# Optimization experiments

Measured on AMD Instinct MI355X. Metric: run time of the kernel, lower is better.

## Reference

```python
import jax, jax.numpy as jnp
from jax import lax
import numpy as np

B, T, D, H, K = 16, 1024, 1024, 1024, 2


def setup_inputs() -> dict:
    key = jax.random.key(0)
    k1, k2 = jax.random.split(key, 2)
    inputs = jax.random.normal(k1, (B, T, D), dtype=jnp.float32)
    # small init so tanh/sigmoid gates are not saturated
    conv_w = jax.random.normal(k2, (3 * H, D, K), dtype=jnp.float32) * 0.02
    conv_b = jnp.zeros((3 * H,), dtype=jnp.float32)
    return {"inputs": inputs, "conv_w": conv_w, "conv_b": conv_b, "layer_idx": 0}


def _qrnn_forward(inputs, conv_w, conv_b):
    k = conv_w.shape[-1]
    h = conv_w.shape[0] // 3
    # causal conv1d: pad (k-1) on the left of the time axis
    x = jnp.transpose(inputs, (0, 2, 1))                 # [B, D, T]
    x = jnp.pad(x, ((0, 0), (0, 0), (k - 1, 0)))         # [B, D, T+k-1]
    gates = lax.conv_general_dilated(
        x, conv_w, window_strides=(1,), padding="VALID",
        dimension_numbers=("NCH", "OIH", "NCH"))         # [B, 3H, T]
    gates = jnp.transpose(gates, (0, 2, 1)) + conv_b     # [B, T, 3H]
    Z = jnp.tanh(gates[..., :h])
    F = jax.nn.sigmoid(gates[..., h:2 * h])
    O = jax.nn.sigmoid(gates[..., 2 * h:])

    # fo-pooling recurrence: c_t = f_t * c_{t-1} + (1 - f_t) * z_t, c_0 = 0
    def step(c, zf):
        z, f = zf
        c_ = f * c + (1.0 - f) * z
        return c_, c_

    c0 = jnp.zeros((Z.shape[0], h), dtype=Z.dtype)
    zT = jnp.transpose(Z, (1, 0, 2))                     # [T, B, H]
    fT = jnp.transpose(F, (1, 0, 2))
    _, cT = lax.scan(step, c0, (zT, fT))                 # [T, B, H]
    c_time = jnp.transpose(cT, (1, 0, 2))                # [B, T, H]
    h_time = O * c_time
    return c_time, h_time


def reference(inputs, conv_w, conv_b, layer_idx):
    # layer_idx=0 with state=None, memory=None: no conv_linear memory term,
    # no attention, zero initial cell state.
    return _qrnn_forward(inputs, conv_w, conv_b)
```

## Files before the change

### kernel.cpp

```cpp
#include <hip/hip_runtime.h>

#define BB 16
#define TT 1024
#define DD 1024
#define HH 1024
#define NN 3072
#define KK 2048
#define MM (BB * TT)
#define TP (TT + 1)
#define NCH 32
#define TC  32
#define PLANE (1u << 24)

typedef __attribute__((ext_vector_type(8))) short short8;
typedef __attribute__((ext_vector_type(4))) float float4v;

__device__ __forceinline__ unsigned short f2bf(float f) {
    unsigned int u = __float_as_uint(f);
    u += 0x7fffu + ((u >> 16) & 1u);
    return (unsigned short)(u >> 16);
}
__device__ __forceinline__ float bf2f(unsigned short s) {
    return __uint_as_float(((unsigned int)s) << 16);
}

__device__ __forceinline__ void gload_lds16(const unsigned short* g, unsigned short* l) {
    __builtin_amdgcn_global_load_lds(
        (const __attribute__((address_space(1))) unsigned int*)(g),
        (__attribute__((address_space(3))) unsigned int*)(l),
        16, 0, 0);
}

__global__ __launch_bounds__(256) void pack_x_kernel(const float* __restrict__ x,
                                                     unsigned short* __restrict__ xpad) {
    int i = blockIdx.x * 256 + threadIdx.x;
    int total = BB * TP * (DD / 4);
    if (i >= total) return;
    int d4  = i & (DD / 4 - 1);
    int row = i >> 8;
    int b  = row / TP;
    int tp = row - b * TP;
    float4 v = make_float4(0.f, 0.f, 0.f, 0.f);
    if (tp > 0)
        v = ((const float4*)x)[(((size_t)(b * TT + tp - 1)) << 8) + d4];
    ushort4 r4;
    r4.x = f2bf(v.x); r4.y = f2bf(v.y); r4.z = f2bf(v.z); r4.w = f2bf(v.w);
    *(ushort4*)(xpad + (((size_t)row) << 10) + (d4 << 2)) = r4;
}

__global__ __launch_bounds__(256) void pack_w_kernel(const float* __restrict__ w,
                                                     unsigned short* __restrict__ Bt) {
    int i = blockIdx.x * 256 + threadIdx.x;
    if (i >= NN * DD) return;
    int n = i >> 10, d = i & 1023;
    float2 v = ((const float2*)w)[i];
    Bt[(size_t)n * KK + d]       = f2bf(v.x);
    Bt[(size_t)n * KK + DD + d]  = f2bf(v.y);
}


#define STAGE_TILE(ASN, BSN, KT) do {                                          \
    const int tap_ = (KT) >> 4;                                                \
    const size_t aoff_ = aSrc + (((size_t)tap_) << 10) + (((KT) & 15) << 6);   \
    const size_t boff_ = bSrc + (((size_t)(KT)) << 6);                         \
    gload_lds16(xpad + aoff_,                 (ASN) + ldsStage);               \
    gload_lds16(xpad + aoff_ + (64u << 10),   (ASN) + ldsStage + 4096);        \
    gload_lds16(xpad + aoff_ + (128u << 10),  (ASN) + ldsStage + 8192);        \
    gload_lds16(xpad + aoff_ + (192u << 10),  (ASN) + ldsStage + 12288);       \
    gload_lds16(Btw + boff_,                  (BSN) + ldsStage);               \
    gload_lds16(Btw + boff_ + (64u << 11),    (BSN) + ldsStage + 4096);        \
    gload_lds16(Btw + boff_ + (128u << 11),   (BSN) + ldsStage + 8192);        \
    gload_lds16(Btw + boff_ + (192u << 11),   (BSN) + ldsStage + 12288);       \
} while (0)

#define MFMA16(P, AA, AB, AC, AD) do {                                         \
    __builtin_amdgcn_s_setprio(1);                                             \
    acc[2*(P)  ][0] = __builtin_amdgcn_mfma_f32_16x16x32_bf16(AA, b00, acc[2*(P)  ][0], 0, 0, 0); \
    acc[2*(P)+1][0] = __builtin_amdgcn_mfma_f32_16x16x32_bf16(AB, b00, acc[2*(P)+1][0], 0, 0, 0); \
    acc[2*(P)  ][1] = __builtin_amdgcn_mfma_f32_16x16x32_bf16(AA, b10, acc[2*(P)  ][1], 0, 0, 0); \
    acc[2*(P)+1][1] = __builtin_amdgcn_mfma_f32_16x16x32_bf16(AB, b10, acc[2*(P)+1][1], 0, 0, 0); \
    acc[2*(P)  ][2] = __builtin_amdgcn_mfma_f32_16x16x32_bf16(AA, b20, acc[2*(P)  ][2], 0, 0, 0); \
    acc[2*(P)+1][2] = __builtin_amdgcn_mfma_f32_16x16x32_bf16(AB, b20, acc[2*(P)+1][2], 0, 0, 0); \
    acc[2*(P)  ][3] = __builtin_amdgcn_mfma_f32_16x16x32_bf16(AA, b30, acc[2*(P)  ][3], 0, 0, 0); \
    acc[2*(P)+1][3] = __builtin_amdgcn_mfma_f32_16x16x32_bf16(AB, b30, acc[2*(P)+1][3], 0, 0, 0); \
    acc[2*(P)  ][0] = __builtin_amdgcn_mfma_f32_16x16x32_bf16(AC, b01, acc[2*(P)  ][0], 0, 0, 0); \
    acc[2*(P)+1][0] = __builtin_amdgcn_mfma_f32_16x16x32_bf16(AD, b01, acc[2*(P)+1][0], 0, 0, 0); \
    acc[2*(P)  ][1] = __builtin_amdgcn_mfma_f32_16x16x32_bf16(AC, b11, acc[2*(P)  ][1], 0, 0, 0); \
    acc[2*(P)+1][1] = __builtin_amdgcn_mfma_f32_16x16x32_bf16(AD, b11, acc[2*(P)+1][1], 0, 0, 0); \
    acc[2*(P)  ][2] = __builtin_amdgcn_mfma_f32_16x16x32_bf16(AC, b21, acc[2*(P)  ][2], 0, 0, 0); \
    acc[2*(P)+1][2] = __builtin_amdgcn_mfma_f32_16x16x32_bf16(AD, b21, acc[2*(P)+1][2], 0, 0, 0); \
    acc[2*(P)  ][3] = __builtin_amdgcn_mfma_f32_16x16x32_bf16(AC, b31, acc[2*(P)  ][3], 0, 0, 0); \
    acc[2*(P)+1][3] = __builtin_amdgcn_mfma_f32_16x16x32_bf16(AD, b31, acc[2*(P)+1][3], 0, 0, 0); \
    __builtin_amdgcn_s_setprio(0);                                             \
} while (0)

#define TILE(ASC, BSC, ASN, BSN, KTN, DOSTAGE) do {                            \
    const unsigned short* aP_ = (ASC) + aRowRd;                                \
    const unsigned short* bP_ = (BSC) + bRowRd;                                \
    short8 b00 = *(const short8*)(bP_ +    0 + pch0);                          \
    short8 b10 = *(const short8*)(bP_ + 1024 + pch0);                          \
    short8 b20 = *(const short8*)(bP_ + 2048 + pch0);                          \
    short8 b30 = *(const short8*)(bP_ + 3072 + pch0);                          \
    short8 aAx = *(const short8*)(aP_ +    0 + pch0);                          \
    short8 aBx = *(const short8*)(aP_ + 1024 + pch0);                          \
    short8 b01 = *(const short8*)(bP_ +    0 + pch1);                          \
    short8 b11 = *(const short8*)(bP_ + 1024 + pch1);                          \
    short8 b21 = *(const short8*)(bP_ + 2048 + pch1);                          \
    short8 b31 = *(const short8*)(bP_ + 3072 + pch1);                          \
    short8 aCx = *(const short8*)(aP_ +    0 + pch1);                          \
    short8 aDx = *(const short8*)(aP_ + 1024 + pch1);                          \
    if (DOSTAGE) { STAGE_TILE(ASN, BSN, KTN); }                                \
    MFMA16(0, aAx, aBx, aCx, aDx);                                             \
    aAx = *(const short8*)(aP_ + 2048 + pch0);                                 \
    aBx = *(const short8*)(aP_ + 3072 + pch0);                                 \
    aCx = *(const short8*)(aP_ + 2048 + pch1);                                 \
    aDx = *(const short8*)(aP_ + 3072 + pch1);                                 \
    MFMA16(1, aAx, aBx, aCx, aDx);                                             \
    aAx = *(const short8*)(aP_ + 4096 + pch0);                                 \
    aBx = *(const short8*)(aP_ + 5120 + pch0);                                 \
    aCx = *(const short8*)(aP_ + 4096 + pch1);                                 \
    aDx = *(const short8*)(aP_ + 5120 + pch1);                                 \
    MFMA16(2, aAx, aBx, aCx, aDx);                                             \
    aAx = *(const short8*)(aP_ + 6144 + pch0);                                 \
    aBx = *(const short8*)(aP_ + 7168 + pch0);                                 \
    aCx = *(const short8*)(aP_ + 6144 + pch1);                                 \
    aDx = *(const short8*)(aP_ + 7168 + pch1);                                 \
    MFMA16(3, aAx, aBx, aCx, aDx);                                             \
    __syncthreads();                                                           \
} while (0)

__global__ __launch_bounds__(512, 2) void gemm_gates_kernel(const unsigned short* __restrict__ xpad,
                                                            const unsigned short* __restrict__ Btw,
                                                            const float* __restrict__ bias,
                                                            unsigned short* __restrict__ zT) {
    extern __shared__ unsigned short lds[];
    unsigned short* As0 = lds;
    unsigned short* As1 = lds + 16384;
    unsigned short* Bs0 = lds + 32768;
    unsigned short* Bs1 = lds + 49152;

    const int tid  = threadIdx.x;
    const int lane = tid & 63;
    const int w    = tid >> 6;
    const int wm   = w >> 2;
    const int wn   = w & 3;
    const int mrow = lane & 15;
    const int quad = lane >> 4;

    const int m0 = blockIdx.x << 8;
    const int n0 = blockIdx.y << 8;
    const int bidx = m0 >> 10;
    const int t0   = m0 & 1023;

    const int rr  = tid >> 3;
    const int cc8 = (((tid & 7) ^ (rr & 7)) << 3);
    const size_t aSrc = (((size_t)(bidx * TP + t0 + rr)) << 10) + cc8;
    const size_t bSrc = (((size_t)(n0 + rr)) << 11) + cc8;
    const int ldsStage = (rr << 6) + ((tid & 7) << 3);

    const int pch0 = ((quad ^ (lane & 7)) << 3);
    const int pch1 = (((4 | quad) ^ (lane & 7)) << 3);
    const int aRowRd = ((wm << 7) + mrow) << 6;
    const int bRowRd = ((wn << 6) + mrow) << 6;

    float4v acc[8][4];
#pragma unroll
    for (int i = 0; i < 8; ++i)
#pragma unroll
        for (int j = 0; j < 4; ++j) acc[i][j] = (float4v)0.0f;

    STAGE_TILE(As0, Bs0, 0);
    __syncthreads();

#pragma unroll 1
    for (int jt = 0; jt < 30; jt += 2) {
        TILE(As0, Bs0, As1, Bs1, jt + 1, 1);
        TILE(As1, Bs1, As0, Bs0, jt + 2, 1);
    }
    TILE(As0, Bs0, As1, Bs1, 31, 1);
    TILE(As1, Bs1, As0, Bs0, 0, 0);

    unsigned short* Ts = lds;
    const bool isZ = (n0 < HH);
    float bv[4];
#pragma unroll
    for (int ng = 0; ng < 4; ++ng) bv[ng] = bias[n0 + (wn << 6) + (ng << 4) + mrow];

#pragma unroll
    for (int g = 0; g < 8; ++g) {
#pragma unroll
        for (int ng = 0; ng < 4; ++ng) {
            const int nloc = (wn << 6) + (ng << 4) + mrow;
            const int m0l  = (wm << 7) + (g << 4) + (quad << 2);
            float v0 = acc[g][ng][0] + bv[ng];
            float v1 = acc[g][ng][1] + bv[ng];
            float v2 = acc[g][ng][2] + bv[ng];
            float v3 = acc[g][ng][3] + bv[ng];
            float g0, g1, g2, g3;
            if (isZ) {
                g0 = 2.0f * __builtin_amdgcn_rcpf(1.0f + __expf(-2.0f * v0)) - 1.0f;
                g1 = 2.0f * __builtin_amdgcn_rcpf(1.0f + __expf(-2.0f * v1)) - 1.0f;
                g2 = 2.0f * __builtin_amdgcn_rcpf(1.0f + __expf(-2.0f * v2)) - 1.0f;
                g3 = 2.0f * __builtin_amdgcn_rcpf(1.0f + __expf(-2.0f * v3)) - 1.0f;
            } else {
                g0 = __builtin_amdgcn_rcpf(1.0f + __expf(-v0));
                g1 = __builtin_amdgcn_rcpf(1.0f + __expf(-v1));
                g2 = __builtin_amdgcn_rcpf(1.0f + __expf(-v2));
                g3 = __builtin_amdgcn_rcpf(1.0f + __expf(-v3));
            }
            unsigned int d0 = (unsigned int)f2bf(g0) | ((unsigned int)f2bf(g1) << 16);
            unsigned int d1 = (unsigned int)f2bf(g2) | ((unsigned int)f2bf(g3) << 16);
            const int chunk = (m0l >> 3) ^ (nloc & 31);
            *(uint2*)(Ts + nloc * 256 + (chunk << 3) + (m0l & 7)) = make_uint2(d0, d1);
        }
    }
    __syncthreads();

    const int gate = n0 >> 10;
    unsigned short* plane = zT + ((size_t)gate << 24);
    const int cl = lane & 31;
#pragma unroll
    for (int p = 0; p < 16; ++p) {
        const int np = (p << 4) + (tid >> 5);
        short8 vv = *(const short8*)(Ts + np * 256 + ((cl ^ (np & 31)) << 3));
        const int h = (n0 & 1023) + np;
        const size_t dst = ((((size_t)((bidx << 10) | h)) << 10) | (unsigned)(t0 + (cl << 3)));
        *(short8*)(plane + dst) = vv;
    }
}


__global__ __launch_bounds__(256) void scan_summary_kernel(const unsigned short* __restrict__ zT,
                                                           float* __restrict__ P,
                                                           float* __restrict__ S) {
    int g = blockIdx.x * 256 + threadIdx.x;
    int h = g & 1023;
    int b = (g >> 10) & 15;
    int j = g >> 14;
    const unsigned short* zp = zT + ((((size_t)((b << 10) | h)) << 10) + j * TC);
    const unsigned short* fp = zp + PLANE;
    short8 zv[4], fv[4];
#pragma unroll
    for (int q = 0; q < 4; ++q) {
        zv[q] = *(const short8*)(zp + q * 8);
        fv[q] = *(const short8*)(fp + q * 8);
    }
    float c = 0.f, pr = 1.f;
#pragma unroll
    for (int q = 0; q < 4; ++q)
#pragma unroll
        for (int k = 0; k < 8; ++k) {
            float z = bf2f((unsigned short)zv[q][k]);
            float f = bf2f((unsigned short)fv[q][k]);
            c = fmaf(f, c, (1.0f - f) * z);
            pr *= f;
        }
    int o = (j << 14) | (b << 10) | h;
    P[o] = pr;
    S[o] = c;
}

__global__ __launch_bounds__(256) void scan_prefix_kernel(const float* __restrict__ P,
                                                          const float* __restrict__ S,
                                                          float* __restrict__ Cin) {
    int idx = blockIdx.x * 256 + threadIdx.x;
    float c = 0.f;
#pragma unroll
    for (int j = 0; j < NCH; ++j) {
        int o = (j << 14) + idx;
        Cin[o] = c;
        c = fmaf(P[o], c, S[o]);
    }
}

__global__ __launch_bounds__(256) void scan_apply_kernel(const unsigned short* __restrict__ zT,
                                                         const float* __restrict__ Cin,
                                                         float* __restrict__ out) {
    int g = blockIdx.x * 256 + threadIdx.x;
    int h = g & 1023;
    int b = (g >> 10) & 15;
    int j = g >> 14;
    const unsigned short* zp = zT + ((((size_t)((b << 10) | h)) << 10) + j * TC);
    const unsigned short* fp = zp + PLANE;
    const unsigned short* op = zp + 2 * (size_t)PLANE;
    short8 zv[4], fv[4], ov[4];
#pragma unroll
    for (int q = 0; q < 4; ++q) {
        zv[q] = *(const short8*)(zp + q * 8);
        fv[q] = *(const short8*)(fp + q * 8);
        ov[q] = *(const short8*)(op + q * 8);
    }
    float c = Cin[(j << 14) | (b << 10) | h];
    float* cbase = out + ((((size_t)((b << 10) | (j * TC))) << 10) | h);
#pragma unroll
    for (int q = 0; q < 4; ++q)
#pragma unroll
        for (int k = 0; k < 8; ++k) {
            float z = bf2f((unsigned short)zv[q][k]);
            float f = bf2f((unsigned short)fv[q][k]);
            float o = bf2f((unsigned short)ov[q][k]);
            c = fmaf(f, c, (1.0f - f) * z);
            float* cp = cbase + (((size_t)(q * 8 + k)) << 10);
            cp[0] = c;
            cp[(size_t)1 << 24] = o * c;
        }
}

extern "C" void kernel_launch(void* const* d_in, const int* in_sizes, int n_in,
                              void* d_out, int out_size, void* d_ws, size_t ws_size,
                              hipStream_t stream) {
    const float* x    = (const float*)d_in[0];
    const float* w    = (const float*)d_in[1];
    const float* bias = (const float*)d_in[2];
    float* out = (float*)d_out;

    char* ws = (char*)d_ws;
    const size_t xpad_bytes = (size_t)BB * TP * DD * 2;
    const size_t btw_bytes  = (size_t)NN * KK * 2;
    unsigned short* xpad = (unsigned short*)ws;
    unsigned short* Btw  = (unsigned short*)(ws + xpad_bytes);
    unsigned short* zT   = (unsigned short*)(ws + xpad_bytes + btw_bytes);
    float* P   = (float*)ws;
    float* S   = (float*)(ws + (size_t)MM * NCH * 4);
    float* Cin = (float*)(ws + (size_t)MM * NCH * 8);

    {
        int total = BB * TP * (DD / 4);
        pack_x_kernel<<<(total + 255) / 256, 256, 0, stream>>>(x, xpad);
    }
    {
        int total = NN * DD;
        pack_w_kernel<<<(total + 255) / 256, 256, 0, stream>>>(w, Btw);
    }
    {
        static int gemm_attr_done = 0;
        if (!gemm_attr_done) {
            (void)hipFuncSetAttribute((const void*)gemm_gates_kernel,
                                      hipFuncAttributeMaxDynamicSharedMemorySize, 131072);
            gemm_attr_done = 1;
        }
        dim3 grid(MM / 256, NN / 256);
        gemm_gates_kernel<<<grid, 512, 131072, stream>>>(xpad, Btw, bias, zT);
    }
    scan_summary_kernel<<<MM * NCH / 256, 256, 0, stream>>>(zT, P, S);
    scan_prefix_kernel<<<MM / 256, 256, 0, stream>>>(P, S, Cin);
    scan_apply_kernel<<<MM * NCH / 256, 256, 0, stream>>>(zT, Cin, out);
}
```

Baseline: 449.6 us.

## Interleave split A/B global-to-LDS staging with MFMA phases using fine-grained barriers

Restructures the GEMM main loop so A and B tile loads are split into halves and issued between the four MFMA phases. B is prefetched two tiles ahead while A is one ahead, and explicit s_waitcnt plus s_barrier calls replace the single end-of-tile __syncthreads. The aim is to spread memory traffic across the compute phases and hide load latency better. The cost is many more barriers per tile, and the hand-tuned waitcnt values and the in-place B buffer overwrite depend on exact load counts, so a miscount would cause races.

```diff
diff --git a/kernel.cpp b/kernel.cpp
--- a/kernel.cpp
+++ b/kernel.cpp
@@ -59,18 +59,20 @@
 }
 
 
-#define STAGE_TILE(ASN, BSN, KT) do {                                          \
-    const int tap_ = (KT) >> 4;                                                \
-    const size_t aoff_ = aSrc + (((size_t)tap_) << 10) + (((KT) & 15) << 6);   \
-    const size_t boff_ = bSrc + (((size_t)(KT)) << 6);                         \
-    gload_lds16(xpad + aoff_,                 (ASN) + ldsStage);               \
-    gload_lds16(xpad + aoff_ + (64u << 10),   (ASN) + ldsStage + 4096);        \
-    gload_lds16(xpad + aoff_ + (128u << 10),  (ASN) + ldsStage + 8192);        \
-    gload_lds16(xpad + aoff_ + (192u << 10),  (ASN) + ldsStage + 12288);       \
-    gload_lds16(Btw + boff_,                  (BSN) + ldsStage);               \
-    gload_lds16(Btw + boff_ + (64u << 11),    (BSN) + ldsStage + 4096);        \
-    gload_lds16(Btw + boff_ + (128u << 11),   (BSN) + ldsStage + 8192);        \
-    gload_lds16(Btw + boff_ + (192u << 11),   (BSN) + ldsStage + 12288);       \
+#define CFENCE asm volatile("" ::: "memory")
+
+#define STAGE_A_HALF(ASN, KT, HALF) do {                                       \
+    const int tapA_ = (KT) >> 4;                                               \
+    const size_t aoffA_ = aSrc + (((size_t)tapA_) << 10) + (((KT) & 15) << 6)  \
+                        + (((size_t)(HALF)) << 17);                            \
+    gload_lds16(xpad + aoffA_,               (ASN) + (HALF) * 8192 + ldsStage);        \
+    gload_lds16(xpad + aoffA_ + (64u << 10), (ASN) + (HALF) * 8192 + ldsStage + 4096); \
+} while (0)
+
+#define STAGE_B_HALF(BSN, KT, HALF) do {                                       \
+    const size_t boffB_ = bSrc + (((size_t)(KT)) << 6) + (((size_t)(HALF)) << 18); \
+    gload_lds16(Btw + boffB_,               (BSN) + (HALF) * 8192 + ldsStage);        \
+    gload_lds16(Btw + boffB_ + (64u << 11), (BSN) + (HALF) * 8192 + ldsStage + 4096); \
 } while (0)
 
 #define MFMA16(P, AA, AB, AC, AD) do {                                         \
@@ -94,39 +96,57 @@
     __builtin_amdgcn_s_setprio(0);                                             \
 } while (0)
 
-#define TILE(ASC, BSC, ASN, BSN, KTN, DOSTAGE) do {                            \
-    const unsigned short* aP_ = (ASC) + aRowRd;                                \
-    const unsigned short* bP_ = (BSC) + bRowRd;                                \
+#define TILE8(AC_, BC_, AN_, T) do {                                           \
+    const int kA_ = ((T) + 1 < 32) ? ((T) + 1) : 31;                           \
+    const int kB_ = ((T) + 2 < 32) ? ((T) + 2) : 31;                           \
+    const unsigned short* aP_ = (AC_) + aRowRd;                                \
+    const unsigned short* bP_ = (BC_) + bRowRd;                                \
+                                                        \
     short8 b00 = *(const short8*)(bP_ +    0 + pch0);                          \
     short8 b10 = *(const short8*)(bP_ + 1024 + pch0);                          \
     short8 b20 = *(const short8*)(bP_ + 2048 + pch0);                          \
     short8 b30 = *(const short8*)(bP_ + 3072 + pch0);                          \
-    short8 aAx = *(const short8*)(aP_ +    0 + pch0);                          \
-    short8 aBx = *(const short8*)(aP_ + 1024 + pch0);                          \
     short8 b01 = *(const short8*)(bP_ +    0 + pch1);                          \
     short8 b11 = *(const short8*)(bP_ + 1024 + pch1);                          \
     short8 b21 = *(const short8*)(bP_ + 2048 + pch1);                          \
     short8 b31 = *(const short8*)(bP_ + 3072 + pch1);                          \
+    short8 aAx = *(const short8*)(aP_ +    0 + pch0);                          \
+    short8 aBx = *(const short8*)(aP_ + 1024 + pch0);                          \
     short8 aCx = *(const short8*)(aP_ +    0 + pch1);                          \
     short8 aDx = *(const short8*)(aP_ + 1024 + pch1);                          \
-    if (DOSTAGE) { STAGE_TILE(ASN, BSN, KTN); }                                \
+    STAGE_A_HALF(AN_, kA_, 0);                                                 \
+    STAGE_A_HALF(AN_, kA_, 1);                                                 \
+    asm volatile("s_waitcnt lgkmcnt(8)" ::: "memory");                         \
+    CFENCE; __builtin_amdgcn_s_barrier(); CFENCE;                              \
     MFMA16(0, aAx, aBx, aCx, aDx);                                             \
+    CFENCE; __builtin_amdgcn_s_barrier(); CFENCE;                              \
+                                                        \
     aAx = *(const short8*)(aP_ + 2048 + pch0);                                 \
     aBx = *(const short8*)(aP_ + 3072 + pch0);                                 \
     aCx = *(const short8*)(aP_ + 2048 + pch1);                                 \
     aDx = *(const short8*)(aP_ + 3072 + pch1);                                 \
+    STAGE_B_HALF(BC_, kB_, 0);                                                 \
+    CFENCE; __builtin_amdgcn_s_barrier(); CFENCE;                              \
     MFMA16(1, aAx, aBx, aCx, aDx);                                             \
+    CFENCE; __builtin_amdgcn_s_barrier(); CFENCE;                              \
+                                                        \
     aAx = *(const short8*)(aP_ + 4096 + pch0);                                 \
     aBx = *(const short8*)(aP_ + 5120 + pch0);                                 \
     aCx = *(const short8*)(aP_ + 4096 + pch1);                                 \
     aDx = *(const short8*)(aP_ + 5120 + pch1);                                 \
+    STAGE_B_HALF(BC_, kB_, 1);                                                 \
+    CFENCE; __builtin_amdgcn_s_barrier(); CFENCE;                              \
     MFMA16(2, aAx, aBx, aCx, aDx);                                             \
+    CFENCE; __builtin_amdgcn_s_barrier(); CFENCE;                              \
+                                                        \
     aAx = *(const short8*)(aP_ + 6144 + pch0);                                 \
     aBx = *(const short8*)(aP_ + 7168 + pch0);                                 \
     aCx = *(const short8*)(aP_ + 6144 + pch1);                                 \
     aDx = *(const short8*)(aP_ + 7168 + pch1);                                 \
+    asm volatile("s_waitcnt vmcnt(4)" ::: "memory");                           \
+    CFENCE; __builtin_amdgcn_s_barrier(); CFENCE;                              \
     MFMA16(3, aAx, aBx, aCx, aDx);                                             \
-    __syncthreads();                                                           \
+    CFENCE; __builtin_amdgcn_s_barrier(); CFENCE;                              \
 } while (0)
 
 __global__ __launch_bounds__(512, 2) void gemm_gates_kernel(const unsigned short* __restrict__ xpad,
@@ -169,16 +189,21 @@
 #pragma unroll
         for (int j = 0; j < 4; ++j) acc[i][j] = (float4v)0.0f;
 
-    STAGE_TILE(As0, Bs0, 0);
+    STAGE_B_HALF(Bs0, 0, 0);
+    STAGE_B_HALF(Bs0, 0, 1);
+    STAGE_A_HALF(As0, 0, 0);
+    STAGE_A_HALF(As0, 0, 1);
+    STAGE_B_HALF(Bs1, 1, 0);
+    STAGE_B_HALF(Bs1, 1, 1);
+    asm volatile("s_waitcnt vmcnt(4)" ::: "memory");
+    CFENCE; __builtin_amdgcn_s_barrier(); CFENCE;
+
+#pragma unroll 1
+    for (int t = 0; t < 32; t += 2) {
+        TILE8(As0, Bs0, As1, t);
+        TILE8(As1, Bs1, As0, t + 1);
+    }
     __syncthreads();
-
-#pragma unroll 1
-    for (int jt = 0; jt < 30; jt += 2) {
-        TILE(As0, Bs0, As1, Bs1, jt + 1, 1);
-        TILE(As1, Bs1, As0, Bs0, jt + 2, 1);
-    }
-    TILE(As0, Bs0, As1, Bs1, 31, 1);
-    TILE(As1, Bs1, As0, Bs0, 0, 0);
 
     unsigned short* Ts = lds;
     const bool isZ = (n0 < HH);
```

After: 443.6 us. Within noise of the previous version (-1.3%).

## Reshape gate storage into 8-step time blocks and parallelize chunk prefix scan

Applied to the files above, without the earlier changes.

The GEMM epilogue now writes gates in a [b][t/8][h][8] layout, so adjacent scan threads read contiguous 16-byte blocks with coalesced access. The scan uses 128 chunks of 8 steps instead of 32 chunks of 32, which raises parallelism and lowers per-thread register use in the summary and apply kernels. The chunk prefix is now computed by a wave-level shuffle scan plus shared memory instead of a sequential loop. The cost is more P/S/Cin traffic, a larger prefix grid, and an extra sync.

```diff
diff --git a/kernel.cpp b/kernel.cpp
--- a/kernel.cpp
+++ b/kernel.cpp
@@ -8,8 +8,8 @@
 #define KK 2048
 #define MM (BB * TT)
 #define TP (TT + 1)
-#define NCH 32
-#define TC  32
+#define NCH 128
+#define TC  8
 #define PLANE (1u << 24)
 
 typedef __attribute__((ext_vector_type(8))) short short8;
@@ -218,13 +218,16 @@
 
     const int gate = n0 >> 10;
     unsigned short* plane = zT + ((size_t)gate << 24);
-    const int cl = lane & 31;
+    const int hl = tid & 255;
+    const int jw = tid >> 8;
+    const int j80 = t0 >> 3;
 #pragma unroll
     for (int p = 0; p < 16; ++p) {
-        const int np = (p << 4) + (tid >> 5);
-        short8 vv = *(const short8*)(Ts + np * 256 + ((cl ^ (np & 31)) << 3));
-        const int h = (n0 & 1023) + np;
-        const size_t dst = ((((size_t)((bidx << 10) | h)) << 10) | (unsigned)(t0 + (cl << 3)));
+        const int j8l = (p << 1) + jw;
+        const int chunk = j8l ^ (hl & 31);
+        short8 vv = *(const short8*)(Ts + hl * 256 + (chunk << 3));
+        const int h = (n0 & 1023) + hl;
+        const size_t dst = ((((size_t)((bidx << 7) | (j80 + j8l))) << 10 | (unsigned)h) << 3);
         *(short8*)(plane + dst) = vv;
     }
 }
@@ -234,27 +237,19 @@
                                                            float* __restrict__ P,
                                                            float* __restrict__ S) {
     int g = blockIdx.x * 256 + threadIdx.x;
-    int h = g & 1023;
-    int b = (g >> 10) & 15;
-    int j = g >> 14;
-    const unsigned short* zp = zT + ((((size_t)((b << 10) | h)) << 10) + j * TC);
+    const unsigned short* zp = zT + ((size_t)g << 3);
     const unsigned short* fp = zp + PLANE;
-    short8 zv[4], fv[4];
-#pragma unroll
-    for (int q = 0; q < 4; ++q) {
-        zv[q] = *(const short8*)(zp + q * 8);
-        fv[q] = *(const short8*)(fp + q * 8);
-    }
+    short8 zv = *(const short8*)zp;
+    short8 fv = *(const short8*)fp;
     float c = 0.f, pr = 1.f;
 #pragma unroll
-    for (int q = 0; q < 4; ++q)
-#pragma unroll
-        for (int k = 0; k < 8; ++k) {
-            float z = bf2f((unsigned short)zv[q][k]);
-            float f = bf2f((unsigned short)fv[q][k]);
-            c = fmaf(f, c, (1.0f - f) * z);
-            pr *= f;
-        }
+    for (int k = 0; k < 8; ++k) {
+        float z = bf2f((unsigned short)zv[k]);
+        float f = bf2f((unsigned short)fv[k]);
+        c = fmaf(f, c, (1.0f - f) * z);
+        pr *= f;
+    }
+    int h = g & 1023, j = (g >> 10) & 127, b = g >> 17;
     int o = (j << 14) | (b << 10) | h;
     P[o] = pr;
     S[o] = c;
@@ -263,47 +258,56 @@
 __global__ __launch_bounds__(256) void scan_prefix_kernel(const float* __restrict__ P,
                                                           const float* __restrict__ S,
                                                           float* __restrict__ Cin) {
-    int idx = blockIdx.x * 256 + threadIdx.x;
-    float c = 0.f;
-#pragma unroll
-    for (int j = 0; j < NCH; ++j) {
-        int o = (j << 14) + idx;
-        Cin[o] = c;
-        c = fmaf(P[o], c, S[o]);
-    }
+    __shared__ float totP[4], totS[4], incl[256];
+    const int tid  = threadIdx.x;
+    const int j    = tid & 127;
+    const int cL   = tid >> 7;
+    const int idx  = blockIdx.x * 2 + cL;
+    const int o    = (j << 14) + idx;
+    const int lane = tid & 63;
+    const int wid  = tid >> 6;
+
+    float p = P[o], s = S[o];
+#pragma unroll
+    for (int d = 1; d < 64; d <<= 1) {
+        float ps = __shfl_up(p, d, 64);
+        float ss = __shfl_up(s, d, 64);
+        if (lane >= d) { s = fmaf(p, ss, s); p = p * ps; }
+    }
+    if (lane == 63) { totP[wid] = p; totS[wid] = s; }
+    __syncthreads();
+    if (wid & 1) {
+        float ss = totS[wid - 1];
+        s = fmaf(p, ss, s);
+    }
+    incl[tid] = s;
+    __syncthreads();
+    Cin[o] = (j == 0) ? 0.f : incl[tid - 1];
 }
 
 __global__ __launch_bounds__(256) void scan_apply_kernel(const unsigned short* __restrict__ zT,
                                                          const float* __restrict__ Cin,
                                                          float* __restrict__ out) {
     int g = blockIdx.x * 256 + threadIdx.x;
-    int h = g & 1023;
-    int b = (g >> 10) & 15;
-    int j = g >> 14;
-    const unsigned short* zp = zT + ((((size_t)((b << 10) | h)) << 10) + j * TC);
+    const unsigned short* zp = zT + ((size_t)g << 3);
     const unsigned short* fp = zp + PLANE;
     const unsigned short* op = zp + 2 * (size_t)PLANE;
-    short8 zv[4], fv[4], ov[4];
-#pragma unroll
-    for (int q = 0; q < 4; ++q) {
-        zv[q] = *(const short8*)(zp + q * 8);
-        fv[q] = *(const short8*)(fp + q * 8);
-        ov[q] = *(const short8*)(op + q * 8);
-    }
+    short8 zv = *(const short8*)zp;
+    short8 fv = *(const short8*)fp;
+    short8 ov = *(const short8*)op;
+    int h = g & 1023, j = (g >> 10) & 127, b = g >> 17;
     float c = Cin[(j << 14) | (b << 10) | h];
     float* cbase = out + ((((size_t)((b << 10) | (j * TC))) << 10) | h);
 #pragma unroll
-    for (int q = 0; q < 4; ++q)
-#pragma unroll
-        for (int k = 0; k < 8; ++k) {
-            float z = bf2f((unsigned short)zv[q][k]);
-            float f = bf2f((unsigned short)fv[q][k]);
-            float o = bf2f((unsigned short)ov[q][k]);
-            c = fmaf(f, c, (1.0f - f) * z);
-            float* cp = cbase + (((size_t)(q * 8 + k)) << 10);
-            cp[0] = c;
-            cp[(size_t)1 << 24] = o * c;
-        }
+    for (int k = 0; k < 8; ++k) {
+        float z = bf2f((unsigned short)zv[k]);
+        float f = bf2f((unsigned short)fv[k]);
+        float o = bf2f((unsigned short)ov[k]);
+        c = fmaf(f, c, (1.0f - f) * z);
+        float* cp = cbase + (((size_t)k) << 10);
+        cp[0] = c;
+        cp[(size_t)1 << 24] = o * c;
+    }
 }
 
 extern "C" void kernel_launch(void* const* d_in, const int* in_sizes, int n_in,
@@ -343,6 +347,6 @@
         gemm_gates_kernel<<<grid, 512, 131072, stream>>>(xpad, Btw, bias, zT);
     }
     scan_summary_kernel<<<MM * NCH / 256, 256, 0, stream>>>(zT, P, S);
-    scan_prefix_kernel<<<MM / 256, 256, 0, stream>>>(P, S, Cin);
+    scan_prefix_kernel<<<MM / 2, 256, 0, stream>>>(P, S, Cin);
     scan_apply_kernel<<<MM * NCH / 256, 256, 0, stream>>>(zT, Cin, out);
 }
```

Result: no change. 440.9 us (-1.9%).
